# Optimization experiments

Measured on AMD Instinct MI355X. Metric: run time of the kernel, lower is better.

The kernel has to match this reference:

```python
import jax, jax.numpy as jnp
import numpy as np

N = 50000
E = 800000
IN_DIM = 512
HID = 256
LAT = 128
K = 10
ALPHA = 0.1
BN_EPS = 1e-5


def setup_inputs() -> dict:
    key = jax.random.key(0)
    ks = jax.random.split(key, 6)
    x = jax.random.normal(ks[0], (N, IN_DIM), dtype=jnp.float32)
    edge_index = jax.random.randint(ks[1], (2, E), 0, N, dtype=jnp.int64)
    W_proj = jax.random.normal(ks[2], (IN_DIM, LAT), dtype=jnp.float32) * (IN_DIM ** -0.5)
    W1 = jax.random.normal(ks[3], (LAT, HID), dtype=jnp.float32) * (LAT ** -0.5)
    W2 = jax.random.normal(ks[4], (HID, LAT), dtype=jnp.float32) * (HID ** -0.5)
    return {
        "x": x, "edge_index": edge_index, "W_proj": W_proj,
        "W1": W1, "b1": jnp.zeros((HID,), jnp.float32),
        "gamma1": jnp.ones((HID,), jnp.float32), "beta1": jnp.zeros((HID,), jnp.float32),
        "mean1": jnp.zeros((HID,), jnp.float32), "var1": jnp.ones((HID,), jnp.float32),
        "W2": W2, "b2": jnp.zeros((LAT,), jnp.float32),
        "gamma2": jnp.ones((LAT,), jnp.float32), "beta2": jnp.zeros((LAT,), jnp.float32),
        "mean2": jnp.zeros((LAT,), jnp.float32), "var2": jnp.ones((LAT,), jnp.float32),
    }


def _gcn_norm(edge_index, n):
    # add self-loops, symmetric normalization D^-1/2 A D^-1/2 (PyG gcn_norm)
    loops = jnp.arange(n, dtype=edge_index.dtype)
    src = jnp.concatenate([edge_index[0], loops])
    dst = jnp.concatenate([edge_index[1], loops])
    deg = jax.ops.segment_sum(jnp.ones_like(dst, jnp.float32), dst, num_segments=n)
    dinv = jax.lax.rsqrt(jnp.maximum(deg, 1.0))  # deg >= 1 with self-loops
    norm = dinv[src] * dinv[dst]
    return src, dst, norm


def _propagate(h, src, dst, norm, n):
    # gather -> scale -> scatter-add: out[dst] += norm * h[src]
    return jax.ops.segment_sum(h[src] * norm[:, None], dst, num_segments=n)


def _bn(h, gamma, beta, mean, var):
    # BatchNorm1d in eval mode (running stats)
    return (h - mean) * jax.lax.rsqrt(var + BN_EPS) * gamma + beta


def reference(x, edge_index, W_proj, W1, b1, gamma1, beta1, mean1, var1,
              W2, b2, gamma2, beta2, mean2, var2):
    n = x.shape[0]
    src, dst, norm = _gcn_norm(edge_index, n)

    z0 = x @ W_proj                                   # [N, LAT]
    h1 = _propagate(z0 @ W1, src, dst, norm, n) + b1  # GCNConv 1
    h1 = jax.nn.relu(_bn(h1, gamma1, beta1, mean1, var1))
    h2 = _propagate(h1 @ W2, src, dst, norm, n) + b2  # GCNConv 2
    h2 = jax.nn.relu(_bn(h2, gamma2, beta2, mean2, var2))

    # APPNP: h_k = (1-alpha) * A_hat h_{k-1} + alpha * h_0
    def step(h, _):
        h = (1.0 - ALPHA) * _propagate(h, src, dst, norm, n) + ALPHA * h2
        return h, None
    z_refined, _ = jax.lax.scan(step, h2, None, length=K)

    z = z_refined + z0
    row, col = edge_index[0], edge_index[1]
    adj = jax.nn.sigmoid(jnp.sum(z[row] * z[col], axis=1))  # [E]
    return adj, z
```

## Files before the change

kernel.cpp:

```cpp
#include <hip/hip_runtime.h>

#define N_NODES 50000
#define N_EDGES 800000
#define IN_DIM  512
#define HID     256
#define LAT     128
#define K_ITERS 10
#define BN_EPS  1e-5f

typedef __attribute__((ext_vector_type(8))) short bf16x8;
typedef __attribute__((ext_vector_type(4))) float f32x4;

__device__ inline float bflo(unsigned v) { return __builtin_bit_cast(float, v << 16); }
__device__ inline float bfhi(unsigned v) { return __builtin_bit_cast(float, v & 0xffff0000u); }
__device__ inline unsigned f2bf_bits(float f)
{
    unsigned u = __builtin_bit_cast(unsigned, f);
    return (u + 0x7fffu + ((u >> 16) & 1u)) >> 16;
}
__device__ inline unsigned packbf(float x, float y)
{
    return f2bf_bits(x) | (f2bf_bits(y) << 16);
}

__global__ void detect_dtype_kernel(const int* __restrict__ ei32, int* __restrict__ flag)
{
    __shared__ int any;
    if (threadIdx.x == 0) any = 0;
    __syncthreads();
    int local = 0;
    for (int i = threadIdx.x; i < 4096; i += blockDim.x)
        local |= ei32[2 * i + 1];
    if (local) atomicOr(&any, 1);
    __syncthreads();
    if (threadIdx.x == 0) flag[0] = (any != 0) ? 1 : 0;
}

__global__ void init_cnt_kernel(int* __restrict__ cnt, int n)
{
    int i = blockIdx.x * blockDim.x + threadIdx.x;
    if (i < n) cnt[i] = 1;
}

__global__ void convert_count_kernel(const void* __restrict__ ei, const int* __restrict__ flag,
                                     int* __restrict__ srcE, int* __restrict__ dstE,
                                     int* __restrict__ cnt, int E)
{
    int e = blockIdx.x * blockDim.x + threadIdx.x;
    if (e >= E) return;
    int s, d;
    if (*flag) {
        const int* p = (const int*)ei;
        s = p[e]; d = p[E + e];
    } else {
        const long long* p = (const long long*)ei;
        s = (int)p[e]; d = (int)p[E + e];
    }
    srcE[e] = s;
    dstE[e] = d;
    atomicAdd(&cnt[d], 1);
}

__global__ __launch_bounds__(256) void block_sum_kernel(const int* __restrict__ cnt,
                                                        int* __restrict__ bsum, int n)
{
    __shared__ int s[256];
    int i = blockIdx.x * 256 + threadIdx.x;
    s[threadIdx.x] = (i < n) ? cnt[i] : 0;
    __syncthreads();
    for (int off = 128; off > 0; off >>= 1) {
        if (threadIdx.x < off) s[threadIdx.x] += s[threadIdx.x + off];
        __syncthreads();
    }
    if (threadIdx.x == 0) bsum[blockIdx.x] = s[0];
}

__global__ __launch_bounds__(256) void block_scan_kernel(int* __restrict__ bsum, int nb)
{
    __shared__ int s[256];
    int t = threadIdx.x;
    int v = (t < nb) ? bsum[t] : 0;
    s[t] = v;
    __syncthreads();
    for (int off = 1; off < 256; off <<= 1) {
        int u = (t >= off) ? s[t - off] : 0;
        __syncthreads();
        s[t] += u;
        __syncthreads();
    }
    if (t < nb) bsum[t] = s[t] - v;
}

__global__ __launch_bounds__(256) void final_scan_kernel(const int* __restrict__ cnt,
                                                         const int* __restrict__ bsum,
                                                         int* __restrict__ rowoff,
                                                         int* __restrict__ cursor,
                                                         float* __restrict__ dinv, int n)
{
    __shared__ int s[256];
    int t = threadIdx.x;
    int i = blockIdx.x * 256 + t;
    int c = (i < n) ? cnt[i] : 0;
    s[t] = c;
    __syncthreads();
    for (int off = 1; off < 256; off <<= 1) {
        int u = (t >= off) ? s[t - off] : 0;
        __syncthreads();
        s[t] += u;
        __syncthreads();
    }
    if (i < n) {
        int excl = bsum[blockIdx.x] + s[t] - c;
        rowoff[i] = excl;
        cursor[i] = excl;
        dinv[i] = rsqrtf((float)c);
    }
    if (i == 0) rowoff[n] = N_EDGES + N_NODES;
}

__global__ void scatter_kernel(const int* __restrict__ srcE, const int* __restrict__ dstE,
                               const float* __restrict__ dinv, int* __restrict__ cursor,
                               uint2* __restrict__ csr, int E, int n)
{
    int e = blockIdx.x * blockDim.x + threadIdx.x;
    if (e >= E + n) return;
    int s, d;
    if (e < E) { s = srcE[e]; d = dstE[e]; }
    else       { s = e - E;   d = s; }
    int pos = atomicAdd(&cursor[d], 1);
    float w = dinv[s] * dinv[d];
    csr[pos] = make_uint2((unsigned)s, __builtin_bit_cast(unsigned, w));
}

__global__ void transpose_cvt_tile(const float* __restrict__ in, unsigned short* __restrict__ out,
                                   int K, int C)
{
    int idx = blockIdx.x * 256 + threadIdx.x;
    if (idx >= K * C) return;
    int k = idx / C, col = idx - k * C;
    int dst = (col >> 7) * (K * 128) + (k >> 3) * 1024 + ((col & 127) << 3) + (k & 7);
    out[dst] = (unsigned short)f2bf_bits(in[idx]);
}

template<int KDIM, int EPI, bool AF32>
__global__ __launch_bounds__(256) void gemm_lds(const void* __restrict__ Ain,
                                                const unsigned short* __restrict__ Bt,
                                                unsigned short* __restrict__ Cout,
                                                int M, int Nc,
                                                const float* __restrict__ cb,
                                                const float* __restrict__ cg,
                                                const float* __restrict__ cbe,
                                                const float* __restrict__ cm,
                                                const float* __restrict__ cv)
{
    constexpr int BK = 64;
    constexpr int NC = KDIM / BK;
    __shared__ unsigned short Bl[BK * 128];
    const int tid  = threadIdx.x;
    const int wave = tid >> 6;
    const int lane = tid & 63;
    const int s  = lane & 15;
    const int kc = lane >> 4;
    const int wrow0   = blockIdx.y * 64 + wave * 16;
    const int colbase = blockIdx.x * 128;
    int arow = wrow0 + s; if (arow > M - 1) arow = M - 1;

    const float*          Af   = (const float*)Ain + (size_t)arow * KDIM + 8 * kc;
    const unsigned short* Ahp  = (const unsigned short*)Ain + (size_t)arow * KDIM + 8 * kc;
    const unsigned short* Bblk = Bt + (size_t)blockIdx.x * KDIM * 128;

    float4 Arf[2][2][2];
    bf16x8 Arh[2][2];
    uint4  Bst[4];
    f32x4  acc[8] = {};

    {
        const uint4* src = (const uint4*)(Bblk + tid * 32);
        Bst[0] = src[0]; Bst[1] = src[1]; Bst[2] = src[2]; Bst[3] = src[3];
    }
#pragma unroll
    for (int kk = 0; kk < 2; ++kk) {
        if constexpr (AF32) {
            Arf[0][kk][0] = *(const float4*)(Af + 32 * kk);
            Arf[0][kk][1] = *(const float4*)(Af + 32 * kk + 4);
        } else {
            Arh[0][kk] = *(const bf16x8*)(Ahp + 32 * kk);
        }
    }
    {
        uint4* d = (uint4*)&Bl[tid * 32];
        d[0] = Bst[0]; d[1] = Bst[1]; d[2] = Bst[2]; d[3] = Bst[3];
    }
    __syncthreads();

#pragma unroll
    for (int c = 0; c < NC; ++c) {
        if (c + 1 < NC) {
            const uint4* src = (const uint4*)(Bblk + (c + 1) * 8192 + tid * 32);
            Bst[0] = src[0]; Bst[1] = src[1]; Bst[2] = src[2]; Bst[3] = src[3];
#pragma unroll
            for (int kk = 0; kk < 2; ++kk) {
                if constexpr (AF32) {
                    Arf[(c + 1) & 1][kk][0] = *(const float4*)(Af + (c + 1) * 64 + 32 * kk);
                    Arf[(c + 1) & 1][kk][1] = *(const float4*)(Af + (c + 1) * 64 + 32 * kk + 4);
                } else {
                    Arh[(c + 1) & 1][kk] = *(const bf16x8*)(Ahp + (c + 1) * 64 + 32 * kk);
                }
            }
        }
#pragma unroll
        for (int kk = 0; kk < 2; ++kk) {
            bf16x8 af;
            if constexpr (AF32) {
                float4 u0 = Arf[c & 1][kk][0];
                float4 u1 = Arf[c & 1][kk][1];
                af[0] = (short)f2bf_bits(u0.x); af[1] = (short)f2bf_bits(u0.y);
                af[2] = (short)f2bf_bits(u0.z); af[3] = (short)f2bf_bits(u0.w);
                af[4] = (short)f2bf_bits(u1.x); af[5] = (short)f2bf_bits(u1.y);
                af[6] = (short)f2bf_bits(u1.z); af[7] = (short)f2bf_bits(u1.w);
            } else {
                af = Arh[c & 1][kk];
            }
#pragma unroll
            for (int t = 0; t < 8; ++t) {
                bf16x8 bf = *(const bf16x8*)&Bl[((kk * 4 + kc) * 128 + t * 16 + s) * 8];
                acc[t] = __builtin_amdgcn_mfma_f32_16x16x32_bf16(af, bf, acc[t], 0, 0, 0);
            }
        }
        __syncthreads();
        if (c + 1 < NC) {
            uint4* d = (uint4*)&Bl[tid * 32];
            d[0] = Bst[0]; d[1] = Bst[1]; d[2] = Bst[2]; d[3] = Bst[3];
            __syncthreads();
        }
    }

#pragma unroll
    for (int t = 0; t < 8; ++t) {
        const int col = colbase + t * 16 + s;
        float sc = 1.f, sh = 0.f;
        if (EPI == 1) {
            sc = cg[col] * rsqrtf(cv[col] + BN_EPS);
            sh = (cb[col] - cm[col]) * sc + cbe[col];
        }
#pragma unroll
        for (int j = 0; j < 4; ++j) {
            const int crow = wrow0 + kc * 4 + j;
            if (crow < M) {
                float xv = acc[t][j];
                if (EPI == 1) xv = fmaxf(fmaf(xv, sc, sh), 0.f);
                Cout[(size_t)crow * Nc + col] = (unsigned short)f2bf_bits(xv);
            }
        }
    }
}

template<int MODE>
__global__ __launch_bounds__(256) void prop_row(const unsigned* __restrict__ in,
                                                const int* __restrict__ rowoff,
                                                const unsigned long long* __restrict__ csr,
                                                const unsigned* __restrict__ h2h,
                                                const unsigned* __restrict__ z0h,
                                                float* __restrict__ outf,
                                                unsigned* __restrict__ outh,
                                                const float* __restrict__ bb,
                                                const float* __restrict__ bg,
                                                const float* __restrict__ bbe,
                                                const float* __restrict__ bm,
                                                const float* __restrict__ bv)
{
    const int node = blockIdx.x * 4 + (threadIdx.x >> 6);
    const int lane = threadIdx.x & 63;
    const int g = lane >> 4, s = lane & 15;
    const int e0 = rowoff[node], e1 = rowoff[node + 1];

    float f[8] = {};
    int e = e0 + g;
    while (e < e1) {
        unsigned long long P[6];
        uint4 V[6];
#pragma unroll
        for (int i = 0; i < 6; ++i) { P[i] = 0; V[i] = make_uint4(0u, 0u, 0u, 0u); }
#pragma unroll
        for (int i = 0; i < 6; ++i)
            if (e + 4 * i < e1) P[i] = csr[e + 4 * i];
#pragma unroll
        for (int i = 0; i < 6; ++i)
            if (e + 4 * i < e1) V[i] = *(const uint4*)&in[(size_t)(unsigned)P[i] * 64 + 4 * s];
#pragma unroll
        for (int i = 0; i < 6; ++i) {
            const float w = __builtin_bit_cast(float, (unsigned)(P[i] >> 32));
            f[0] = fmaf(w, bflo(V[i].x), f[0]); f[1] = fmaf(w, bfhi(V[i].x), f[1]);
            f[2] = fmaf(w, bflo(V[i].y), f[2]); f[3] = fmaf(w, bfhi(V[i].y), f[3]);
            f[4] = fmaf(w, bflo(V[i].z), f[4]); f[5] = fmaf(w, bfhi(V[i].z), f[5]);
            f[6] = fmaf(w, bflo(V[i].w), f[6]); f[7] = fmaf(w, bfhi(V[i].w), f[7]);
        }
        e += 24;
    }
#pragma unroll
    for (int i = 0; i < 8; ++i) {
        f[i] += __shfl_xor(f[i], 16, 64);
        f[i] += __shfl_xor(f[i], 32, 64);
    }

    if (g == 0) {
        const size_t o = (size_t)node * 64 + 4 * s;
        uint4 ov;
        if (MODE == 0) {
            ov.x = packbf(f[0], f[1]); ov.y = packbf(f[2], f[3]);
            ov.z = packbf(f[4], f[5]); ov.w = packbf(f[6], f[7]);
            *(uint4*)&outh[o] = ov;
        } else if (MODE == 1) {
            float4 G0 = *(const float4*)&bg[8 * s],  G1 = *(const float4*)&bg[8 * s + 4];
            float4 V0 = *(const float4*)&bv[8 * s],  V1 = *(const float4*)&bv[8 * s + 4];
            float4 B0 = *(const float4*)&bb[8 * s],  B1 = *(const float4*)&bb[8 * s + 4];
            float4 M0 = *(const float4*)&bm[8 * s],  M1 = *(const float4*)&bm[8 * s + 4];
            float4 E0 = *(const float4*)&bbe[8 * s], E1 = *(const float4*)&bbe[8 * s + 4];
            float gg[8] = {G0.x, G0.y, G0.z, G0.w, G1.x, G1.y, G1.z, G1.w};
            float vv[8] = {V0.x, V0.y, V0.z, V0.w, V1.x, V1.y, V1.z, V1.w};
            float bbv[8] = {B0.x, B0.y, B0.z, B0.w, B1.x, B1.y, B1.z, B1.w};
            float mm[8] = {M0.x, M0.y, M0.z, M0.w, M1.x, M1.y, M1.z, M1.w};
            float ee[8] = {E0.x, E0.y, E0.z, E0.w, E1.x, E1.y, E1.z, E1.w};
            float r[8];
#pragma unroll
            for (int i = 0; i < 8; ++i) {
                float sc = gg[i] * rsqrtf(vv[i] + BN_EPS);
                float sh = (bbv[i] - mm[i]) * sc + ee[i];
                r[i] = fmaxf(fmaf(f[i], sc, sh), 0.f);
            }
            ov.x = packbf(r[0], r[1]); ov.y = packbf(r[2], r[3]);
            ov.z = packbf(r[4], r[5]); ov.w = packbf(r[6], r[7]);
            *(uint4*)&outh[o] = ov;
        } else if (MODE == 2) {
            uint4 hv = *(const uint4*)&h2h[o];
            ov.x = packbf(fmaf(0.9f, f[0], 0.1f * bflo(hv.x)), fmaf(0.9f, f[1], 0.1f * bfhi(hv.x)));
            ov.y = packbf(fmaf(0.9f, f[2], 0.1f * bflo(hv.y)), fmaf(0.9f, f[3], 0.1f * bfhi(hv.y)));
            ov.z = packbf(fmaf(0.9f, f[4], 0.1f * bflo(hv.z)), fmaf(0.9f, f[5], 0.1f * bfhi(hv.z)));
            ov.w = packbf(fmaf(0.9f, f[6], 0.1f * bflo(hv.w)), fmaf(0.9f, f[7], 0.1f * bfhi(hv.w)));
            *(uint4*)&outh[o] = ov;
        } else {
            uint4 hv = *(const uint4*)&h2h[o];
            uint4 zv = *(const uint4*)&z0h[o];
            float r[8];
            r[0] = fmaf(0.9f, f[0], 0.1f * bflo(hv.x)) + bflo(zv.x);
            r[1] = fmaf(0.9f, f[1], 0.1f * bfhi(hv.x)) + bfhi(zv.x);
            r[2] = fmaf(0.9f, f[2], 0.1f * bflo(hv.y)) + bflo(zv.y);
            r[3] = fmaf(0.9f, f[3], 0.1f * bfhi(hv.y)) + bfhi(zv.y);
            r[4] = fmaf(0.9f, f[4], 0.1f * bflo(hv.z)) + bflo(zv.z);
            r[5] = fmaf(0.9f, f[5], 0.1f * bfhi(hv.z)) + bfhi(zv.z);
            r[6] = fmaf(0.9f, f[6], 0.1f * bflo(hv.w)) + bflo(zv.w);
            r[7] = fmaf(0.9f, f[7], 0.1f * bfhi(hv.w)) + bfhi(zv.w);
            *(float4*)&outf[(size_t)node * LAT + 8 * s]     = make_float4(r[0], r[1], r[2], r[3]);
            *(float4*)&outf[(size_t)node * LAT + 8 * s + 4] = make_float4(r[4], r[5], r[6], r[7]);
            ov.x = packbf(r[0], r[1]); ov.y = packbf(r[2], r[3]);
            ov.z = packbf(r[4], r[5]); ov.w = packbf(r[6], r[7]);
            *(uint4*)&outh[o] = ov;
        }
    }
}

__global__ __launch_bounds__(256) void edge_dot_mfma(const unsigned* __restrict__ zh,
                                                     const int* __restrict__ srcE,
                                                     const int* __restrict__ dstE,
                                                     float* __restrict__ adj)
{
    const int gw = blockIdx.x * 4 + (threadIdx.x >> 6);
    const int base = gw * 16;
    const int lane = threadIdx.x & 63;
    const int s = lane & 15, kc = lane >> 4;
    const int r = srcE[base + s];
    const int c = dstE[base + s];
    const unsigned* zr = &zh[(size_t)r * 64 + 4 * kc];
    const unsigned* zc = &zh[(size_t)c * 64 + 4 * kc];
    f32x4 acc = {};
#pragma unroll
    for (int k0 = 0; k0 < 4; ++k0) {
        bf16x8 af = *(const bf16x8*)(zr + 16 * k0);
        bf16x8 bf = *(const bf16x8*)(zc + 16 * k0);
        acc = __builtin_amdgcn_mfma_f32_16x16x32_bf16(af, bf, acc, 0, 0, 0);
    }
    if ((s >> 2) == kc) {
        const int j = s & 3;
        float v = (j == 0) ? acc[0] : (j == 1) ? acc[1] : (j == 2) ? acc[2] : acc[3];
        adj[base + s] = 1.f / (1.f + expf(-v));
    }
}

extern "C" void kernel_launch(void* const* d_in, const int* in_sizes, int n_in,
                              void* d_out, int out_size, void* d_ws, size_t ws_size,
                              hipStream_t stream)
{
    const float* x     = (const float*)d_in[0];
    const void*  ei    = d_in[1];
    const float* Wproj = (const float*)d_in[2];
    const float* W1    = (const float*)d_in[3];
    const float* b1    = (const float*)d_in[4];
    const float* g1    = (const float*)d_in[5];
    const float* be1   = (const float*)d_in[6];
    const float* m1    = (const float*)d_in[7];
    const float* v1    = (const float*)d_in[8];
    const float* W2    = (const float*)d_in[9];
    const float* b2    = (const float*)d_in[10];
    const float* g2    = (const float*)d_in[11];
    const float* be2   = (const float*)d_in[12];
    const float* m2    = (const float*)d_in[13];
    const float* v2    = (const float*)d_in[14];

    float* out_adj = (float*)d_out;
    float* out_z   = (float*)d_out + N_EDGES;

    char* w = (char*)d_ws;
    size_t off = 0;
    auto alloc = [&](size_t bytes) {
        void* p = w + off;
        off += (bytes + 255) & ~(size_t)255;
        return p;
    };
    const size_t NB = (size_t)N_NODES * 64 * 4;
    const int NBLK = (N_NODES + 255) / 256;

    int*            flag   = (int*)           alloc(4);
    int*            cnt    = (int*)           alloc((size_t)N_NODES * 4);
    int*            cursor = (int*)           alloc((size_t)N_NODES * 4);
    int*            rowoff = (int*)           alloc((size_t)(N_NODES + 1) * 4);
    float*          dinv   = (float*)         alloc((size_t)N_NODES * 4);
    int*            bsum   = (int*)           alloc(256 * 4);
    int*            srcE   = (int*)           alloc((size_t)N_EDGES * 4);
    int*            dstE   = (int*)           alloc((size_t)N_EDGES * 4);
    uint2*          csr    = (uint2*)         alloc((size_t)(N_EDGES + N_NODES) * 8);
    unsigned short* Wpt    = (unsigned short*)alloc((size_t)LAT * IN_DIM * 2);
    unsigned short* W1t    = (unsigned short*)alloc((size_t)HID * LAT * 2);
    unsigned short* W2t    = (unsigned short*)alloc((size_t)LAT * HID * 2);
    unsigned*       z0h    = (unsigned*)      alloc(NB);
    unsigned*       p0h    = (unsigned*)      alloc(NB);
    unsigned short* h1h    = (unsigned short*)alloc(2 * NB);
    unsigned*       t2h    = (unsigned*)      alloc(NB);
    unsigned*       h2h    = (unsigned*)      alloc(NB);

    unsigned* pingA = (unsigned*)h1h;
    unsigned* pingB = (unsigned*)h1h + N_NODES * 64;

    detect_dtype_kernel<<<1, 256, 0, stream>>>((const int*)ei, flag);
    init_cnt_kernel<<<(N_NODES + 255) / 256, 256, 0, stream>>>(cnt, N_NODES);
    convert_count_kernel<<<(N_EDGES + 255) / 256, 256, 0, stream>>>(ei, flag, srcE, dstE, cnt, N_EDGES);
    block_sum_kernel<<<NBLK, 256, 0, stream>>>(cnt, bsum, N_NODES);
    block_scan_kernel<<<1, 256, 0, stream>>>(bsum, NBLK);
    final_scan_kernel<<<NBLK, 256, 0, stream>>>(cnt, bsum, rowoff, cursor, dinv, N_NODES);
    scatter_kernel<<<(N_EDGES + N_NODES + 255) / 256, 256, 0, stream>>>(srcE, dstE, dinv, cursor,
                                                                        csr, N_EDGES, N_NODES);

    transpose_cvt_tile<<<(IN_DIM * LAT + 255) / 256, 256, 0, stream>>>(Wproj, Wpt, IN_DIM, LAT);
    transpose_cvt_tile<<<(LAT * HID + 255) / 256, 256, 0, stream>>>(W1, W1t, LAT, HID);
    transpose_cvt_tile<<<(HID * LAT + 255) / 256, 256, 0, stream>>>(W2, W2t, HID, LAT);

    const int gy = (N_NODES + 63) / 64;
    const int pgrid = N_NODES / 4;

    gemm_lds<IN_DIM, 0, true><<<dim3(1, gy), 256, 0, stream>>>(x, Wpt, (unsigned short*)z0h,
                                                               N_NODES, LAT,
                                                               nullptr, nullptr, nullptr, nullptr, nullptr);
    prop_row<0><<<pgrid, 256, 0, stream>>>(z0h, rowoff, (const unsigned long long*)csr,
                                           nullptr, nullptr, nullptr, p0h,
                                           nullptr, nullptr, nullptr, nullptr, nullptr);
    gemm_lds<LAT, 1, false><<<dim3(2, gy), 256, 0, stream>>>(p0h, W1t, h1h, N_NODES, HID,
                                                             b1, g1, be1, m1, v1);
    gemm_lds<HID, 0, false><<<dim3(1, gy), 256, 0, stream>>>(h1h, W2t, (unsigned short*)t2h,
                                                             N_NODES, LAT,
                                                             nullptr, nullptr, nullptr, nullptr, nullptr);
    prop_row<1><<<pgrid, 256, 0, stream>>>(t2h, rowoff, (const unsigned long long*)csr,
                                           nullptr, nullptr, nullptr, h2h,
                                           b2, g2, be2, m2, v2);

    const unsigned* cur = h2h;
    for (int it = 0; it < K_ITERS; ++it) {
        if (it == K_ITERS - 1) {
            prop_row<3><<<pgrid, 256, 0, stream>>>(cur, rowoff, (const unsigned long long*)csr,
                                                   h2h, z0h, out_z, z0h,
                                                   nullptr, nullptr, nullptr, nullptr, nullptr);
        } else {
            unsigned* nxt = (it & 1) ? pingB : pingA;
            prop_row<2><<<pgrid, 256, 0, stream>>>(cur, rowoff, (const unsigned long long*)csr,
                                                   h2h, nullptr, nullptr, nxt,
                                                   nullptr, nullptr, nullptr, nullptr, nullptr);
            cur = nxt;
        }
    }

    edge_dot_mfma<<<N_EDGES / 64, 256, 0, stream>>>(z0h, srcE, dstE, out_adj);
}
```

Baseline: 680.2 us.

## Slice feature matrices into 16-column planes and pack CSR entries into 32 bits

Node features are stored as eight column slices of 16 bf16 values each. Each propagation block handles one slice for 16 nodes, so that slice stays small enough to remain cache-resident during the random gathers. CSR entries are packed into 32 bits (16-bit source index plus bf16 weight) and loaded nontemporally, halving edge-list traffic. The packing assumes node ids fit in 16 bits, but N is 50000, so it breaks for larger graphs. The bf16 weight also loses precision, and the edge list is now read eight times, once per slice.

Result: slower. 1.184 ms (+74.1%).

```diff
diff --git a/kernel.cpp b/kernel.cpp
--- a/kernel.cpp
+++ b/kernel.cpp
@@ -120,7 +120,7 @@
 
 __global__ void scatter_kernel(const int* __restrict__ srcE, const int* __restrict__ dstE,
                                const float* __restrict__ dinv, int* __restrict__ cursor,
-                               uint2* __restrict__ csr, int E, int n)
+                               unsigned* __restrict__ csr, int E, int n)
 {
     int e = blockIdx.x * blockDim.x + threadIdx.x;
     if (e >= E + n) return;
@@ -129,7 +129,7 @@
     else       { s = e - E;   d = s; }
     int pos = atomicAdd(&cursor[d], 1);
     float w = dinv[s] * dinv[d];
-    csr[pos] = make_uint2((unsigned)s, __builtin_bit_cast(unsigned, w));
+    csr[pos] = (unsigned)s | (f2bf_bits(w) << 16);
 }
 
 __global__ void transpose_cvt_tile(const float* __restrict__ in, unsigned short* __restrict__ out,
@@ -142,7 +142,7 @@
     out[dst] = (unsigned short)f2bf_bits(in[idx]);
 }
 
-template<int KDIM, int EPI, bool AF32>
+template<int KDIM, int EPI, bool AF32, int OUT>
 __global__ __launch_bounds__(256) void gemm_lds(const void* __restrict__ Ain,
                                                 const unsigned short* __restrict__ Bt,
                                                 unsigned short* __restrict__ Cout,
@@ -249,47 +249,54 @@
             if (crow < M) {
                 float xv = acc[t][j];
                 if (EPI == 1) xv = fmaxf(fmaf(xv, sc, sh), 0.f);
-                Cout[(size_t)crow * Nc + col] = (unsigned short)f2bf_bits(xv);
+                if (OUT == 1)
+                    Cout[(size_t)t * (N_NODES * 16) + (size_t)crow * 16 + s] = (unsigned short)f2bf_bits(xv);
+                else
+                    Cout[(size_t)crow * Nc + col] = (unsigned short)f2bf_bits(xv);
             }
         }
     }
 }
 
 template<int MODE>
-__global__ __launch_bounds__(256) void prop_row(const unsigned* __restrict__ in,
-                                                const int* __restrict__ rowoff,
-                                                const unsigned long long* __restrict__ csr,
-                                                const unsigned* __restrict__ h2h,
-                                                const unsigned* __restrict__ z0h,
-                                                float* __restrict__ outf,
-                                                unsigned* __restrict__ outh,
-                                                const float* __restrict__ bb,
-                                                const float* __restrict__ bg,
-                                                const float* __restrict__ bbe,
-                                                const float* __restrict__ bm,
-                                                const float* __restrict__ bv)
-{
-    const int node = blockIdx.x * 4 + (threadIdx.x >> 6);
+__global__ __launch_bounds__(256) void prop_slice(const unsigned* __restrict__ in,
+                                                  const int* __restrict__ rowoff,
+                                                  const unsigned* __restrict__ csr,
+                                                  const unsigned* __restrict__ h2h,
+                                                  const unsigned* __restrict__ z0h,
+                                                  float* __restrict__ outf,
+                                                  unsigned* __restrict__ outh,
+                                                  const float* __restrict__ bb,
+                                                  const float* __restrict__ bg,
+                                                  const float* __restrict__ bbe,
+                                                  const float* __restrict__ bm,
+                                                  const float* __restrict__ bv)
+{
+    const int q    = blockIdx.x & 7;
+    const int nb   = blockIdx.x >> 3;
+    const int wave = threadIdx.x >> 6;
     const int lane = threadIdx.x & 63;
-    const int g = lane >> 4, s = lane & 15;
+    const int node = nb * 16 + wave * 4 + (lane >> 4);
+    const int u = lane & 15, g = u >> 1, p = u & 1;
     const int e0 = rowoff[node], e1 = rowoff[node + 1];
+    const unsigned* inq = in + (size_t)q * (N_NODES * 8);
 
     float f[8] = {};
     int e = e0 + g;
     while (e < e1) {
-        unsigned long long P[6];
-        uint4 V[6];
-#pragma unroll
-        for (int i = 0; i < 6; ++i) { P[i] = 0; V[i] = make_uint4(0u, 0u, 0u, 0u); }
-#pragma unroll
-        for (int i = 0; i < 6; ++i)
-            if (e + 4 * i < e1) P[i] = csr[e + 4 * i];
-#pragma unroll
-        for (int i = 0; i < 6; ++i)
-            if (e + 4 * i < e1) V[i] = *(const uint4*)&in[(size_t)(unsigned)P[i] * 64 + 4 * s];
-#pragma unroll
-        for (int i = 0; i < 6; ++i) {
-            const float w = __builtin_bit_cast(float, (unsigned)(P[i] >> 32));
+        unsigned P[3];
+        uint4 V[3];
+#pragma unroll
+        for (int i = 0; i < 3; ++i) { P[i] = 0; V[i] = make_uint4(0u, 0u, 0u, 0u); }
+#pragma unroll
+        for (int i = 0; i < 3; ++i)
+            if (e + 8 * i < e1) P[i] = __builtin_nontemporal_load(&csr[e + 8 * i]);
+#pragma unroll
+        for (int i = 0; i < 3; ++i)
+            if (e + 8 * i < e1) V[i] = *(const uint4*)&inq[(size_t)(P[i] & 0xFFFFu) * 8 + p * 4];
+#pragma unroll
+        for (int i = 0; i < 3; ++i) {
+            const float w = __builtin_bit_cast(float, P[i] & 0xffff0000u);
             f[0] = fmaf(w, bflo(V[i].x), f[0]); f[1] = fmaf(w, bfhi(V[i].x), f[1]);
             f[2] = fmaf(w, bflo(V[i].y), f[2]); f[3] = fmaf(w, bfhi(V[i].y), f[3]);
             f[4] = fmaf(w, bflo(V[i].z), f[4]); f[5] = fmaf(w, bfhi(V[i].z), f[5]);
@@ -299,23 +306,25 @@
     }
 #pragma unroll
     for (int i = 0; i < 8; ++i) {
-        f[i] += __shfl_xor(f[i], 16, 64);
-        f[i] += __shfl_xor(f[i], 32, 64);
-    }
-
-    if (g == 0) {
-        const size_t o = (size_t)node * 64 + 4 * s;
+        f[i] += __shfl_xor(f[i], 2, 64);
+        f[i] += __shfl_xor(f[i], 4, 64);
+        f[i] += __shfl_xor(f[i], 8, 64);
+    }
+
+    if (u < 2) {
+        const size_t so = (size_t)q * (N_NODES * 8) + (size_t)node * 8 + p * 4;
         uint4 ov;
         if (MODE == 0) {
             ov.x = packbf(f[0], f[1]); ov.y = packbf(f[2], f[3]);
             ov.z = packbf(f[4], f[5]); ov.w = packbf(f[6], f[7]);
-            *(uint4*)&outh[o] = ov;
+            *(uint4*)&outh[(size_t)node * 64 + q * 8 + p * 4] = ov;
         } else if (MODE == 1) {
-            float4 G0 = *(const float4*)&bg[8 * s],  G1 = *(const float4*)&bg[8 * s + 4];
-            float4 V0 = *(const float4*)&bv[8 * s],  V1 = *(const float4*)&bv[8 * s + 4];
-            float4 B0 = *(const float4*)&bb[8 * s],  B1 = *(const float4*)&bb[8 * s + 4];
-            float4 M0 = *(const float4*)&bm[8 * s],  M1 = *(const float4*)&bm[8 * s + 4];
-            float4 E0 = *(const float4*)&bbe[8 * s], E1 = *(const float4*)&bbe[8 * s + 4];
+            const int d0 = q * 16 + p * 8;
+            float4 G0 = *(const float4*)&bg[d0],  G1 = *(const float4*)&bg[d0 + 4];
+            float4 V0 = *(const float4*)&bv[d0],  V1 = *(const float4*)&bv[d0 + 4];
+            float4 B0 = *(const float4*)&bb[d0],  B1 = *(const float4*)&bb[d0 + 4];
+            float4 M0 = *(const float4*)&bm[d0],  M1 = *(const float4*)&bm[d0 + 4];
+            float4 E0 = *(const float4*)&bbe[d0], E1 = *(const float4*)&bbe[d0 + 4];
             float gg[8] = {G0.x, G0.y, G0.z, G0.w, G1.x, G1.y, G1.z, G1.w};
             float vv[8] = {V0.x, V0.y, V0.z, V0.w, V1.x, V1.y, V1.z, V1.w};
             float bbv[8] = {B0.x, B0.y, B0.z, B0.w, B1.x, B1.y, B1.z, B1.w};
@@ -330,17 +339,17 @@
             }
             ov.x = packbf(r[0], r[1]); ov.y = packbf(r[2], r[3]);
             ov.z = packbf(r[4], r[5]); ov.w = packbf(r[6], r[7]);
-            *(uint4*)&outh[o] = ov;
+            *(uint4*)&outh[so] = ov;
         } else if (MODE == 2) {
-            uint4 hv = *(const uint4*)&h2h[o];
+            uint4 hv = *(const uint4*)&h2h[so];
             ov.x = packbf(fmaf(0.9f, f[0], 0.1f * bflo(hv.x)), fmaf(0.9f, f[1], 0.1f * bfhi(hv.x)));
             ov.y = packbf(fmaf(0.9f, f[2], 0.1f * bflo(hv.y)), fmaf(0.9f, f[3], 0.1f * bfhi(hv.y)));
             ov.z = packbf(fmaf(0.9f, f[4], 0.1f * bflo(hv.z)), fmaf(0.9f, f[5], 0.1f * bfhi(hv.z)));
             ov.w = packbf(fmaf(0.9f, f[6], 0.1f * bflo(hv.w)), fmaf(0.9f, f[7], 0.1f * bfhi(hv.w)));
-            *(uint4*)&outh[o] = ov;
+            *(uint4*)&outh[so] = ov;
         } else {
-            uint4 hv = *(const uint4*)&h2h[o];
-            uint4 zv = *(const uint4*)&z0h[o];
+            uint4 hv = *(const uint4*)&h2h[so];
+            uint4 zv = *(const uint4*)&z0h[so];
             float r[8];
             r[0] = fmaf(0.9f, f[0], 0.1f * bflo(hv.x)) + bflo(zv.x);
             r[1] = fmaf(0.9f, f[1], 0.1f * bfhi(hv.x)) + bfhi(zv.x);
@@ -350,11 +359,11 @@
             r[5] = fmaf(0.9f, f[5], 0.1f * bfhi(hv.z)) + bfhi(zv.z);
             r[6] = fmaf(0.9f, f[6], 0.1f * bflo(hv.w)) + bflo(zv.w);
             r[7] = fmaf(0.9f, f[7], 0.1f * bfhi(hv.w)) + bfhi(zv.w);
-            *(float4*)&outf[(size_t)node * LAT + 8 * s]     = make_float4(r[0], r[1], r[2], r[3]);
-            *(float4*)&outf[(size_t)node * LAT + 8 * s + 4] = make_float4(r[4], r[5], r[6], r[7]);
+            *(float4*)&outf[(size_t)node * LAT + q * 16 + p * 8]     = make_float4(r[0], r[1], r[2], r[3]);
+            *(float4*)&outf[(size_t)node * LAT + q * 16 + p * 8 + 4] = make_float4(r[4], r[5], r[6], r[7]);
             ov.x = packbf(r[0], r[1]); ov.y = packbf(r[2], r[3]);
             ov.z = packbf(r[4], r[5]); ov.w = packbf(r[6], r[7]);
-            *(uint4*)&outh[o] = ov;
+            *(uint4*)&outh[so] = ov;
         }
     }
 }
@@ -370,13 +379,12 @@
     const int s = lane & 15, kc = lane >> 4;
     const int r = srcE[base + s];
     const int c = dstE[base + s];
-    const unsigned* zr = &zh[(size_t)r * 64 + 4 * kc];
-    const unsigned* zc = &zh[(size_t)c * 64 + 4 * kc];
     f32x4 acc = {};
 #pragma unroll
     for (int k0 = 0; k0 < 4; ++k0) {
-        bf16x8 af = *(const bf16x8*)(zr + 16 * k0);
-        bf16x8 bf = *(const bf16x8*)(zc + 16 * k0);
+        const size_t so = (size_t)(2 * k0 + (kc >> 1)) * (N_NODES * 8) + (kc & 1) * 4;
+        bf16x8 af = *(const bf16x8*)&zh[so + (size_t)r * 8];
+        bf16x8 bf = *(const bf16x8*)&zh[so + (size_t)c * 8];
         acc = __builtin_amdgcn_mfma_f32_16x16x32_bf16(af, bf, acc, 0, 0, 0);
     }
     if ((s >> 2) == kc) {
@@ -427,7 +435,7 @@
     int*            bsum   = (int*)           alloc(256 * 4);
     int*            srcE   = (int*)           alloc((size_t)N_EDGES * 4);
     int*            dstE   = (int*)           alloc((size_t)N_EDGES * 4);
-    uint2*          csr    = (uint2*)         alloc((size_t)(N_EDGES + N_NODES) * 8);
+    unsigned*       csr    = (unsigned*)      alloc((size_t)(N_EDGES + N_NODES) * 4);
     unsigned short* Wpt    = (unsigned short*)alloc((size_t)LAT * IN_DIM * 2);
     unsigned short* W1t    = (unsigned short*)alloc((size_t)HID * LAT * 2);
     unsigned short* W2t    = (unsigned short*)alloc((size_t)LAT * HID * 2);
@@ -454,34 +462,30 @@
     transpose_cvt_tile<<<(HID * LAT + 255) / 256, 256, 0, stream>>>(W2, W2t, HID, LAT);
 
     const int gy = (N_NODES + 63) / 64;
-    const int pgrid = N_NODES / 4;
-
-    gemm_lds<IN_DIM, 0, true><<<dim3(1, gy), 256, 0, stream>>>(x, Wpt, (unsigned short*)z0h,
-                                                               N_NODES, LAT,
-                                                               nullptr, nullptr, nullptr, nullptr, nullptr);
-    prop_row<0><<<pgrid, 256, 0, stream>>>(z0h, rowoff, (const unsigned long long*)csr,
-                                           nullptr, nullptr, nullptr, p0h,
-                                           nullptr, nullptr, nullptr, nullptr, nullptr);
-    gemm_lds<LAT, 1, false><<<dim3(2, gy), 256, 0, stream>>>(p0h, W1t, h1h, N_NODES, HID,
-                                                             b1, g1, be1, m1, v1);
-    gemm_lds<HID, 0, false><<<dim3(1, gy), 256, 0, stream>>>(h1h, W2t, (unsigned short*)t2h,
-                                                             N_NODES, LAT,
-                                                             nullptr, nullptr, nullptr, nullptr, nullptr);
-    prop_row<1><<<pgrid, 256, 0, stream>>>(t2h, rowoff, (const unsigned long long*)csr,
-                                           nullptr, nullptr, nullptr, h2h,
-                                           b2, g2, be2, m2, v2);
+    const int pgrid = (N_NODES / 16) * 8;
+
+    gemm_lds<IN_DIM, 0, true, 1><<<dim3(1, gy), 256, 0, stream>>>(x, Wpt, (unsigned short*)z0h,
+                                                                  N_NODES, LAT,
+                                                                  nullptr, nullptr, nullptr, nullptr, nullptr);
+    prop_slice<0><<<pgrid, 256, 0, stream>>>(z0h, rowoff, csr, nullptr, nullptr, nullptr, p0h,
+                                             nullptr, nullptr, nullptr, nullptr, nullptr);
+    gemm_lds<LAT, 1, false, 0><<<dim3(2, gy), 256, 0, stream>>>(p0h, W1t, h1h, N_NODES, HID,
+                                                                b1, g1, be1, m1, v1);
+    gemm_lds<HID, 0, false, 1><<<dim3(1, gy), 256, 0, stream>>>(h1h, W2t, (unsigned short*)t2h,
+                                                                N_NODES, LAT,
+                                                                nullptr, nullptr, nullptr, nullptr, nullptr);
+    prop_slice<1><<<pgrid, 256, 0, stream>>>(t2h, rowoff, csr, nullptr, nullptr, nullptr, h2h,
+                                             b2, g2, be2, m2, v2);
 
     const unsigned* cur = h2h;
     for (int it = 0; it < K_ITERS; ++it) {
         if (it == K_ITERS - 1) {
-            prop_row<3><<<pgrid, 256, 0, stream>>>(cur, rowoff, (const unsigned long long*)csr,
-                                                   h2h, z0h, out_z, z0h,
-                                                   nullptr, nullptr, nullptr, nullptr, nullptr);
+            prop_slice<3><<<pgrid, 256, 0, stream>>>(cur, rowoff, csr, h2h, z0h, out_z, z0h,
+                                                     nullptr, nullptr, nullptr, nullptr, nullptr);
         } else {
             unsigned* nxt = (it & 1) ? pingB : pingA;
-            prop_row<2><<<pgrid, 256, 0, stream>>>(cur, rowoff, (const unsigned long long*)csr,
-                                                   h2h, nullptr, nullptr, nxt,
-                                                   nullptr, nullptr, nullptr, nullptr, nullptr);
+            prop_slice<2><<<pgrid, 256, 0, stream>>>(cur, rowoff, csr, h2h, nullptr, nullptr, nxt,
+                                                     nullptr, nullptr, nullptr, nullptr, nullptr);
             cur = nxt;
         }
     }
```

## Pack CSR entries into 32 bits and double-buffer GEMM B tiles via direct LDS loads

Applied to the files above, without the earlier changes.

Each CSR entry now packs a 16-bit source index and a bf16 edge weight into one 32-bit word instead of an 8-byte pair. This halves the edge-list traffic in every propagation pass, at the cost of bf16 precision on the normalisation weights and a hard limit of 65536 nodes. The GEMM kernel now stages B tiles straight from global memory into double-buffered LDS with global_load_lds. That removes the register round trip and one barrier per K-chunk, but doubles LDS use and relies on correct waits for the asynchronous LDS writes.

New measurement: 638.8 us. 1.06x faster.

```diff
diff --git a/kernel.cpp b/kernel.cpp
--- a/kernel.cpp
+++ b/kernel.cpp
@@ -21,6 +21,13 @@
 __device__ inline unsigned packbf(float x, float y)
 {
     return f2bf_bits(x) | (f2bf_bits(y) << 16);
+}
+
+__device__ inline void gload_lds16(const unsigned short* g, unsigned short* l)
+{
+    __builtin_amdgcn_global_load_lds(
+        (const __attribute__((address_space(1))) unsigned int*)g,
+        (__attribute__((address_space(3))) unsigned int*)l, 16, 0, 0);
 }
 
 __global__ void detect_dtype_kernel(const int* __restrict__ ei32, int* __restrict__ flag)
@@ -120,7 +127,7 @@
 
 __global__ void scatter_kernel(const int* __restrict__ srcE, const int* __restrict__ dstE,
                                const float* __restrict__ dinv, int* __restrict__ cursor,
-                               uint2* __restrict__ csr, int E, int n)
+                               unsigned* __restrict__ csr, int E, int n)
 {
     int e = blockIdx.x * blockDim.x + threadIdx.x;
     if (e >= E + n) return;
@@ -129,7 +136,7 @@
     else       { s = e - E;   d = s; }
     int pos = atomicAdd(&cursor[d], 1);
     float w = dinv[s] * dinv[d];
-    csr[pos] = make_uint2((unsigned)s, __builtin_bit_cast(unsigned, w));
+    csr[pos] = (unsigned)s | (f2bf_bits(w) << 16);
 }
 
 __global__ void transpose_cvt_tile(const float* __restrict__ in, unsigned short* __restrict__ out,
@@ -155,7 +162,7 @@
 {
     constexpr int BK = 64;
     constexpr int NC = KDIM / BK;
-    __shared__ unsigned short Bl[BK * 128];
+    __shared__ unsigned short Bl[2][BK * 128];
     const int tid  = threadIdx.x;
     const int wave = tid >> 6;
     const int lane = tid & 63;
@@ -171,13 +178,17 @@
 
     float4 Arf[2][2][2];
     bf16x8 Arh[2][2];
-    uint4  Bst[4];
     f32x4  acc[8] = {};
 
-    {
-        const uint4* src = (const uint4*)(Bblk + tid * 32);
-        Bst[0] = src[0]; Bst[1] = src[1]; Bst[2] = src[2]; Bst[3] = src[3];
-    }
+    auto stage = [&](int c, int buf) {
+#pragma unroll
+        for (int i = 0; i < 4; ++i) {
+            const int j = wave * 4 + i;
+            gload_lds16(Bblk + (size_t)c * 8192 + j * 512 + lane * 8, &Bl[buf][j * 512]);
+        }
+    };
+
+    stage(0, 0);
 #pragma unroll
     for (int kk = 0; kk < 2; ++kk) {
         if constexpr (AF32) {
@@ -187,17 +198,12 @@
             Arh[0][kk] = *(const bf16x8*)(Ahp + 32 * kk);
         }
     }
-    {
-        uint4* d = (uint4*)&Bl[tid * 32];
-        d[0] = Bst[0]; d[1] = Bst[1]; d[2] = Bst[2]; d[3] = Bst[3];
-    }
     __syncthreads();
 
 #pragma unroll
     for (int c = 0; c < NC; ++c) {
         if (c + 1 < NC) {
-            const uint4* src = (const uint4*)(Bblk + (c + 1) * 8192 + tid * 32);
-            Bst[0] = src[0]; Bst[1] = src[1]; Bst[2] = src[2]; Bst[3] = src[3];
+            stage(c + 1, (c + 1) & 1);
 #pragma unroll
             for (int kk = 0; kk < 2; ++kk) {
                 if constexpr (AF32) {
@@ -223,16 +229,11 @@
             }
 #pragma unroll
             for (int t = 0; t < 8; ++t) {
-                bf16x8 bf = *(const bf16x8*)&Bl[((kk * 4 + kc) * 128 + t * 16 + s) * 8];
+                bf16x8 bf = *(const bf16x8*)&Bl[c & 1][((kk * 4 + kc) * 128 + t * 16 + s) * 8];
                 acc[t] = __builtin_amdgcn_mfma_f32_16x16x32_bf16(af, bf, acc[t], 0, 0, 0);
             }
         }
         __syncthreads();
-        if (c + 1 < NC) {
-            uint4* d = (uint4*)&Bl[tid * 32];
-            d[0] = Bst[0]; d[1] = Bst[1]; d[2] = Bst[2]; d[3] = Bst[3];
-            __syncthreads();
-        }
     }
 
 #pragma unroll
@@ -258,7 +259,7 @@
 template<int MODE>
 __global__ __launch_bounds__(256) void prop_row(const unsigned* __restrict__ in,
                                                 const int* __restrict__ rowoff,
-                                                const unsigned long long* __restrict__ csr,
+                                                const unsigned* __restrict__ csr,
                                                 const unsigned* __restrict__ h2h,
                                                 const unsigned* __restrict__ z0h,
                                                 float* __restrict__ outf,
@@ -277,7 +278,7 @@
     float f[8] = {};
     int e = e0 + g;
     while (e < e1) {
-        unsigned long long P[6];
+        unsigned P[6];
         uint4 V[6];
 #pragma unroll
         for (int i = 0; i < 6; ++i) { P[i] = 0; V[i] = make_uint4(0u, 0u, 0u, 0u); }
@@ -286,10 +287,10 @@
             if (e + 4 * i < e1) P[i] = csr[e + 4 * i];
 #pragma unroll
         for (int i = 0; i < 6; ++i)
-            if (e + 4 * i < e1) V[i] = *(const uint4*)&in[(size_t)(unsigned)P[i] * 64 + 4 * s];
+            if (e + 4 * i < e1) V[i] = *(const uint4*)&in[(size_t)(P[i] & 0xFFFFu) * 64 + 4 * s];
 #pragma unroll
         for (int i = 0; i < 6; ++i) {
-            const float w = __builtin_bit_cast(float, (unsigned)(P[i] >> 32));
+            const float w = __builtin_bit_cast(float, P[i] & 0xffff0000u);
             f[0] = fmaf(w, bflo(V[i].x), f[0]); f[1] = fmaf(w, bfhi(V[i].x), f[1]);
             f[2] = fmaf(w, bflo(V[i].y), f[2]); f[3] = fmaf(w, bfhi(V[i].y), f[3]);
             f[4] = fmaf(w, bflo(V[i].z), f[4]); f[5] = fmaf(w, bfhi(V[i].z), f[5]);
@@ -427,7 +428,7 @@
     int*            bsum   = (int*)           alloc(256 * 4);
     int*            srcE   = (int*)           alloc((size_t)N_EDGES * 4);
     int*            dstE   = (int*)           alloc((size_t)N_EDGES * 4);
-    uint2*          csr    = (uint2*)         alloc((size_t)(N_EDGES + N_NODES) * 8);
+    unsigned*       csr    = (unsigned*)      alloc((size_t)(N_EDGES + N_NODES) * 4);
     unsigned short* Wpt    = (unsigned short*)alloc((size_t)LAT * IN_DIM * 2);
     unsigned short* W1t    = (unsigned short*)alloc((size_t)HID * LAT * 2);
     unsigned short* W2t    = (unsigned short*)alloc((size_t)LAT * HID * 2);
@@ -459,28 +460,24 @@
     gemm_lds<IN_DIM, 0, true><<<dim3(1, gy), 256, 0, stream>>>(x, Wpt, (unsigned short*)z0h,
                                                                N_NODES, LAT,
                                                                nullptr, nullptr, nullptr, nullptr, nullptr);
-    prop_row<0><<<pgrid, 256, 0, stream>>>(z0h, rowoff, (const unsigned long long*)csr,
-                                           nullptr, nullptr, nullptr, p0h,
+    prop_row<0><<<pgrid, 256, 0, stream>>>(z0h, rowoff, csr, nullptr, nullptr, nullptr, p0h,
                                            nullptr, nullptr, nullptr, nullptr, nullptr);
     gemm_lds<LAT, 1, false><<<dim3(2, gy), 256, 0, stream>>>(p0h, W1t, h1h, N_NODES, HID,
                                                              b1, g1, be1, m1, v1);
     gemm_lds<HID, 0, false><<<dim3(1, gy), 256, 0, stream>>>(h1h, W2t, (unsigned short*)t2h,
                                                              N_NODES, LAT,
                                                              nullptr, nullptr, nullptr, nullptr, nullptr);
-    prop_row<1><<<pgrid, 256, 0, stream>>>(t2h, rowoff, (const unsigned long long*)csr,
-                                           nullptr, nullptr, nullptr, h2h,
+    prop_row<1><<<pgrid, 256, 0, stream>>>(t2h, rowoff, csr, nullptr, nullptr, nullptr, h2h,
                                            b2, g2, be2, m2, v2);
 
     const unsigned* cur = h2h;
     for (int it = 0; it < K_ITERS; ++it) {
         if (it == K_ITERS - 1) {
-            prop_row<3><<<pgrid, 256, 0, stream>>>(cur, rowoff, (const unsigned long long*)csr,
-                                                   h2h, z0h, out_z, z0h,
+            prop_row<3><<<pgrid, 256, 0, stream>>>(cur, rowoff, csr, h2h, z0h, out_z, z0h,
                                                    nullptr, nullptr, nullptr, nullptr, nullptr);
         } else {
             unsigned* nxt = (it & 1) ? pingB : pingA;
-            prop_row<2><<<pgrid, 256, 0, stream>>>(cur, rowoff, (const unsigned long long*)csr,
-                                                   h2h, nullptr, nullptr, nxt,
+            prop_row<2><<<pgrid, 256, 0, stream>>>(cur, rowoff, csr, h2h, nullptr, nullptr, nxt,
                                                    nullptr, nullptr, nullptr, nullptr, nullptr);
             cur = nxt;
         }
```
